# Optimization experiments

Hardware: AMD Instinct MI355X
Metric: run time of the kernel (lower is better)

Reference implementation:

```python
import jax, jax.numpy as jnp
import numpy as np

SLIDING_WINDOW = 512  # matches init kwarg
BLOCK_STRIDE = 32     # tokens per cache page


def setup_inputs() -> dict:
    key = jax.random.key(0)
    k0, k1, k2, k3 = jax.random.split(key, 4)
    B, S, HQ, HKV, D = 2, 2048, 32, 8, 128
    nb = S // BLOCK_STRIDE
    q = jax.random.normal(k0, (B, S, HQ, D), jnp.float32)
    k = jax.random.normal(k1, (B, S, HKV, D), jnp.float32)
    v = jax.random.normal(k2, (B, S, HKV, D), jnp.float32)
    sink = jax.random.normal(k3, (HQ,), jnp.float32)
    cache_state = jnp.zeros((B * nb, 2, HKV, BLOCK_STRIDE, D), jnp.float32)
    seq_block_ids = jnp.arange(B * nb, dtype=jnp.int32).reshape(B, nb)
    return {"q": q, "k": k, "v": v, "cache_state": cache_state,
            "seq_block_ids": seq_block_ids, "sink": sink}


def reference(q, k, v, cache_state, seq_block_ids, sink):
    B, S, HQ, D = q.shape
    HKV = k.shape[2]
    G = HQ // HKV  # GQA group size
    stride = cache_state.shape[3]
    nb = S // stride

    # --- write prefill K/V into the paged cache ---
    # pages laid out [num_pages, k/v, HKV, stride, D]
    k_pg = k.reshape(B, nb, stride, HKV, D).transpose(0, 1, 3, 2, 4).reshape(B * nb, HKV, stride, D)
    v_pg = v.reshape(B, nb, stride, HKV, D).transpose(0, 1, 3, 2, 4).reshape(B * nb, HKV, stride, D)
    ids = seq_block_ids.reshape(-1)
    new_cache = cache_state.at[ids, 0].set(k_pg).at[ids, 1].set(v_pg)

    # --- sliding-window causal attention with sink logits (GQA, no repeat) ---
    scale = 1.0 / np.sqrt(D).astype(np.float32)
    qg = q.reshape(B, S, HKV, G, D)
    # scores: [B, HKV, G, Sq, Sk]
    scores = jnp.einsum('bqhgd,bshd->bhgqs', qg, k) * scale
    i = jnp.arange(S)[:, None]
    j = jnp.arange(S)[None, :]
    allowed = (j <= i) & ((i - j) < SLIDING_WINDOW)  # causal banded mask
    neg = jnp.finfo(scores.dtype).min
    scores = jnp.where(allowed, scores, neg)
    # per-head sink logit appended as extra key column, dropped after softmax
    sink_col = jnp.broadcast_to(sink.reshape(HKV, G)[None, :, :, None, None], (B, HKV, G, S, 1))
    probs = jax.nn.softmax(jnp.concatenate([scores, sink_col], axis=-1), axis=-1)[..., :S]
    out = jnp.einsum('bhgqs,bshd->bqhgd', probs, v).reshape(B, S, HQ, D)
    return out, new_cache
```

## Files before the change

### kernel.cpp

```cpp
#include <hip/hip_runtime.h>
#include <hip/hip_bf16.h>
#include <stdint.h>

#define BB 2
#define SS 2048
#define HQ 32
#define HKV 8
#define DD 128
#define WIN 512

typedef __bf16 bf16x8 __attribute__((ext_vector_type(8)));
typedef __bf16 bf16x4 __attribute__((ext_vector_type(4)));
typedef float f32x4 __attribute__((ext_vector_type(4)));

__device__ __forceinline__ bf16x8 cvt8(float4 a, float4 b, float s) {
  bf16x8 r;
  r[0] = (__bf16)(a.x * s); r[1] = (__bf16)(a.y * s);
  r[2] = (__bf16)(a.z * s); r[3] = (__bf16)(a.w * s);
  r[4] = (__bf16)(b.x * s); r[5] = (__bf16)(b.y * s);
  r[6] = (__bf16)(b.z * s); r[7] = (__bf16)(b.w * s);
  return r;
}

__global__ __launch_bounds__(512, 2) void attn_kernel(
    const float* __restrict__ qg, const float* __restrict__ kg,
    const float* __restrict__ vg, const float* __restrict__ sinkg,
    float* __restrict__ outg)
{
  const int sid = (blockIdx.x & 7) * 64 + (blockIdx.x >> 3);
  const int qtile = sid & 31, hkv = (sid >> 5) & 7, b = sid >> 8;
  const int qb = qtile * 64;
  const int tid = threadIdx.x;
  const int wave = tid >> 6, lane = tid & 63;
  const int wq = wave & 3, wh = wave >> 2;
  const int g = lane >> 4, c = lane & 15;
  const int hq0 = (hkv << 2) + (wh << 1);

  __shared__ __bf16 Kl[2][32 * 128];
  __shared__ __bf16 Vt[2][128 * 40];
  __shared__ __bf16 Pl[16][16 * 40];

  const float LOG2E = 1.4426950408889634f;
  const float scale = 0.08838834764831845f * LOG2E;
  const float THR = 12.0f;
  const int qw = qb + wq * 16;
  const int qrow = qw + c;

  bf16x8 qf[2][4];
  #pragma unroll
  for (int hh = 0; hh < 2; ++hh) {
    const float* qp = qg + (((size_t)b * SS + qrow) * HQ + hq0 + hh) * DD;
    #pragma unroll
    for (int ch = 0; ch < 4; ++ch) {
      float4 a = *(const float4*)(qp + ch * 32 + g * 8);
      float4 b2 = *(const float4*)(qp + ch * 32 + g * 8 + 4);
      qf[hh][ch] = cvt8(a, b2, scale);
    }
  }

  const float sk[2] = {sinkg[hq0] * LOG2E, sinkg[hq0 + 1] * LOG2E};

  float mm[2] = {-1e30f, -1e30f}, ll[2] = {0.f, 0.f};
  f32x4 acc[2][8];
  #pragma unroll
  for (int hh = 0; hh < 2; ++hh)
    #pragma unroll
    for (int i = 0; i < 8; ++i) acc[hh][i] = (f32x4){0.f, 0.f, 0.f, 0.f};

  const int t0 = (qb > (WIN - 1) ? (qb - (WIN - 1)) : 0) >> 5;
  const int t1 = (qb + 63) >> 5;

  const int krow = tid >> 4, kh = tid & 15;
  const int vd = tid & 127, vc4 = tid >> 7;
  const int KSTEP = 32 * HKV * DD;
  const float* kp = kg + (((size_t)b * SS + (t0 << 5) + krow) * HKV + hkv) * DD + kh * 8;
  const float* vp = vg + (((size_t)b * SS + (t0 << 5) + vc4 * 8) * HKV + hkv) * DD + vd;

  float4 ka, ka2; float vr[8];
  auto issue = [&]() {
    ka = *(const float4*)(kp);
    ka2 = *(const float4*)(kp + 4);
    #pragma unroll
    for (int j = 0; j < 8; ++j) vr[j] = vp[(size_t)j * (HKV * DD)];
  };
  auto commit = [&](int buf) {
    *(bf16x8*)((char*)(&Kl[buf][0]) + krow * 256 + ((kh * 16) ^ ((krow & 7) << 4))) =
        cvt8(ka, ka2, 1.f);
    bf16x8 w;
    #pragma unroll
    for (int j = 0; j < 8; ++j) w[j] = (__bf16)vr[j];
    *(bf16x8*)(&Vt[buf][vd * 40 + vc4 * 8]) = w;
  };

  issue();
  commit(0);
  __syncthreads();
  int cur = 0;

  for (int t = t0; t <= t1; ++t) {
    const int kb = t << 5;
    const bool hn = (t < t1);
    if (hn) { kp += KSTEP; vp += KSTEP; issue(); }

    const bool active = !(kb > qw + 15 || kb + 31 < qw - (WIN - 1));
    if (active) {
      const __bf16* Ks = &Kl[cur][0];
      const __bf16* Vs = &Vt[cur][0];

      f32x4 sc0[2] = {{0.f,0.f,0.f,0.f},{0.f,0.f,0.f,0.f}};
      f32x4 sc1[2] = {{0.f,0.f,0.f,0.f},{0.f,0.f,0.f,0.f}};
      #pragma unroll
      for (int ch = 0; ch < 4; ++ch) {
        const int off = (ch * 64 + g * 16) ^ ((c & 7) << 4);
        bf16x8 a0 = *(const bf16x8*)((const char*)Ks + c * 256 + off);
        bf16x8 a1 = *(const bf16x8*)((const char*)Ks + (16 + c) * 256 + off);
        sc0[0] = __builtin_amdgcn_mfma_f32_16x16x32_bf16(a0, qf[0][ch], sc0[0], 0, 0, 0);
        sc1[0] = __builtin_amdgcn_mfma_f32_16x16x32_bf16(a1, qf[0][ch], sc1[0], 0, 0, 0);
        sc0[1] = __builtin_amdgcn_mfma_f32_16x16x32_bf16(a0, qf[1][ch], sc0[1], 0, 0, 0);
        sc1[1] = __builtin_amdgcn_mfma_f32_16x16x32_bf16(a1, qf[1][ch], sc1[1], 0, 0, 0);
      }

      const bool noMask = (kb + 31 <= qw) && (kb >= qw - (WIN - 16));

      #pragma unroll
      for (int hh = 0; hh < 2; ++hh) {
        float p[8];
        #pragma unroll
        for (int r = 0; r < 4; ++r) { p[r] = sc0[hh][r]; p[4 + r] = sc1[hh][r]; }
        if (!noMask) {
          #pragma unroll
          for (int t2 = 0; t2 < 2; ++t2)
            #pragma unroll
            for (int r = 0; r < 4; ++r) {
              const int kk = kb + t2 * 16 + g * 4 + r;
              const bool ok = (kk <= qrow) && (qrow - kk < WIN);
              p[t2 * 4 + r] = ok ? p[t2 * 4 + r] : -1e30f;
            }
        }
        float tmax = p[0];
        #pragma unroll
        for (int j = 1; j < 8; ++j) tmax = fmaxf(tmax, p[j]);
        tmax = fmaxf(tmax, __shfl_xor(tmax, 16));
        tmax = fmaxf(tmax, __shfl_xor(tmax, 32));

        const bool resc = __any(tmax > mm[hh] + THR);
        const float mnew = resc ? fmaxf(mm[hh], tmax) : mm[hh];
        float tsum = 0.f;
        if (noMask) {
          #pragma unroll
          for (int j = 0; j < 8; ++j) { p[j] = exp2f(p[j] - mnew); tsum += p[j]; }
        } else {
          #pragma unroll
          for (int j = 0; j < 8; ++j) {
            const float e = (p[j] > -9e29f) ? exp2f(p[j] - mnew) : 0.f;
            p[j] = e; tsum += e;
          }
        }
        tsum += __shfl_xor(tsum, 16);
        tsum += __shfl_xor(tsum, 32);

        if (resc) {
          const float scl = exp2f(mm[hh] - mnew);
          ll[hh] = ll[hh] * scl + tsum;
          const float f0 = __shfl(scl, g * 4 + 0), f1 = __shfl(scl, g * 4 + 1);
          const float f2 = __shfl(scl, g * 4 + 2), f3 = __shfl(scl, g * 4 + 3);
          #pragma unroll
          for (int dt = 0; dt < 8; ++dt) {
            acc[hh][dt][0] *= f0; acc[hh][dt][1] *= f1;
            acc[hh][dt][2] *= f2; acc[hh][dt][3] *= f3;
          }
          mm[hh] = mnew;
        } else {
          ll[hh] += tsum;
        }

        char* pb = (char*)(&Pl[wave * 2 + hh][0]) + c * 80;
        #pragma unroll
        for (int t2 = 0; t2 < 2; ++t2) {
          bf16x4 w;
          w[0] = (__bf16)p[t2 * 4 + 0]; w[1] = (__bf16)p[t2 * 4 + 1];
          w[2] = (__bf16)p[t2 * 4 + 2]; w[3] = (__bf16)p[t2 * 4 + 3];
          *(bf16x4*)(pb + t2 * 32 + g * 8) = w;
        }
      }

      bf16x8 pa0 = *(bf16x8*)((char*)(&Pl[wave * 2 + 0][0]) + c * 80 + g * 16);
      bf16x8 pa1 = *(bf16x8*)((char*)(&Pl[wave * 2 + 1][0]) + c * 80 + g * 16);
      #pragma unroll
      for (int dt = 0; dt < 8; ++dt) {
        bf16x8 vv = *(const bf16x8*)(Vs + (dt * 16 + c) * 40 + g * 8);
        acc[0][dt] = __builtin_amdgcn_mfma_f32_16x16x32_bf16(pa0, vv, acc[0][dt], 0, 0, 0);
        acc[1][dt] = __builtin_amdgcn_mfma_f32_16x16x32_bf16(pa1, vv, acc[1][dt], 0, 0, 0);
      }
    }

    if (hn) {
      commit(cur ^ 1);
      __syncthreads();
      cur ^= 1;
    }
  }

  #pragma unroll
  for (int hh = 0; hh < 2; ++hh) {
    const float Mf = fmaxf(mm[hh], sk[hh]);
    const float ex = exp2f(mm[hh] - Mf);
    const float denom = ll[hh] * ex + exp2f(sk[hh] - Mf);
    const float fac = ex / denom;
    const float f0 = __shfl(fac, g * 4 + 0), f1 = __shfl(fac, g * 4 + 1);
    const float f2 = __shfl(fac, g * 4 + 2), f3 = __shfl(fac, g * 4 + 3);
    const float fr[4] = {f0, f1, f2, f3};
    #pragma unroll
    for (int dt = 0; dt < 8; ++dt) {
      #pragma unroll
      for (int r = 0; r < 4; ++r) {
        const int row = qw + g * 4 + r;
        outg[(((size_t)b * SS + row) * HQ + hq0 + hh) * DD + dt * 16 + c] = acc[hh][dt][r] * fr[r];
      }
    }
  }
}

__global__ void build_inv(const int* __restrict__ ids, int* __restrict__ inv,
                          int npages, int nslots) {
  const int i = threadIdx.x;
  if (i < npages) inv[i] = -1;
  __syncthreads();
  if (i < nslots) inv[ids[i]] = i;
}

__global__ void page_fill(const float* __restrict__ kg, const float* __restrict__ vg,
                          const float* __restrict__ cache_in, const int* __restrict__ inv,
                          float* __restrict__ cache) {
  const int page = blockIdx.x, half = blockIdx.y;
  const int slot = inv[page];
  float4* d4 = (float4*)cache;
  const size_t dbase = (((size_t)page * 2 + half) * 8) * 1024;
  if (slot >= 0) {
    const int b = slot >> 6, blk = slot & 63;
    const float4* s4 = (const float4*)(half ? vg : kg);
    for (int f = threadIdx.x; f < 8192; f += blockDim.x) {
      const int d = f & 31, s = (f >> 5) & 31, h = f >> 10;
      d4[dbase + (size_t)h * 1024 + s * 32 + d] =
          s4[(((size_t)b * SS + blk * 32 + s) * 8 + h) * 32 + d];
    }
  } else {
    const float4* s4 = (const float4*)cache_in;
    for (int f = threadIdx.x; f < 8192; f += blockDim.x)
      d4[dbase + f] = s4[dbase + f];
  }
}

__global__ void cache_copy(const float* __restrict__ src, float* __restrict__ dst, int n4) {
  const float4* s = (const float4*)src;
  float4* d = (float4*)dst;
  for (int i = blockIdx.x * blockDim.x + threadIdx.x; i < n4; i += gridDim.x * blockDim.x)
    d[i] = s[i];
}
__global__ void cache_scatter(const float* __restrict__ kg, const float* __restrict__ vg,
                              const int* __restrict__ ids, float* __restrict__ cache) {
  const int slot = blockIdx.x;
  const int half = blockIdx.y;
  const int b = slot >> 6, blk = slot & 63;
  const int page = ids[slot];
  const float4* s4 = (const float4*)(half ? vg : kg);
  float4* d4 = (float4*)cache;
  for (int f = threadIdx.x; f < 8192; f += blockDim.x) {
    const int d = f & 31, s = (f >> 5) & 31, h = f >> 10;
    d4[(((size_t)page * 2 + half) * 8 + h) * 1024 + s * 32 + d] =
        s4[(((size_t)b * SS + blk * 32 + s) * 8 + h) * 32 + d];
  }
}

extern "C" void kernel_launch(void* const* d_in, const int* in_sizes, int n_in,
                              void* d_out, int out_size, void* d_ws, size_t ws_size,
                              hipStream_t stream) {
  const float* q = (const float*)d_in[0];
  const float* k = (const float*)d_in[1];
  const float* v = (const float*)d_in[2];
  const float* cache_in = (const float*)d_in[3];
  const int* ids = (const int*)d_in[4];
  const float* sink = (const float*)d_in[5];
  float* out = (float*)d_out;
  float* cache_out = out + (size_t)BB * SS * HQ * DD;

  const int nslots = in_sizes[4];
  const int npages = in_sizes[3] / (2 * HKV * 32 * DD);

  if (ws_size >= (size_t)npages * sizeof(int) && npages <= 1024) {
    int* inv = (int*)d_ws;
    build_inv<<<1, 1024, 0, stream>>>(ids, inv, npages, nslots);
    page_fill<<<dim3(npages, 2), 256, 0, stream>>>(k, v, cache_in, inv, cache_out);
  } else {
    cache_copy<<<4096, 256, 0, stream>>>(cache_in, cache_out, (BB * SS * HKV * DD * 2) / 4);
    cache_scatter<<<dim3(BB * 64, 2), 256, 0, stream>>>(k, v, ids, cache_out);
  }
  attn_kernel<<<512, 512, 0, stream>>>(q, k, v, sink, out);
}
```

Before: 109.9 us.

## Double query tile per block to 128 rows, reuse K/V tiles across two row slabs

```diff
diff --git a/kernel.cpp b/kernel.cpp
--- a/kernel.cpp
+++ b/kernel.cpp
@@ -27,9 +27,9 @@
     const float* __restrict__ vg, const float* __restrict__ sinkg,
     float* __restrict__ outg)
 {
-  const int sid = (blockIdx.x & 7) * 64 + (blockIdx.x >> 3);
-  const int qtile = sid & 31, hkv = (sid >> 5) & 7, b = sid >> 8;
-  const int qb = qtile * 64;
+  const int sid = (blockIdx.x & 7) * 32 + (blockIdx.x >> 3);
+  const int qtile = sid & 15, hkv = (sid >> 4) & 7, b = sid >> 7;
+  const int qb = qtile * 128;
   const int tid = threadIdx.x;
   const int wave = tid >> 6, lane = tid & 63;
   const int wq = wave & 3, wh = wave >> 2;
@@ -38,37 +38,39 @@
 
   __shared__ __bf16 Kl[2][32 * 128];
   __shared__ __bf16 Vt[2][128 * 40];
-  __shared__ __bf16 Pl[16][16 * 40];
+  __shared__ __bf16 Pl[32][16 * 40];
 
   const float LOG2E = 1.4426950408889634f;
   const float scale = 0.08838834764831845f * LOG2E;
   const float THR = 12.0f;
-  const int qw = qb + wq * 16;
-  const int qrow = qw + c;
-
-  bf16x8 qf[2][4];
+  const int qw_lo = qb + wq * 32;
+
+  bf16x8 qf[4][4];
   #pragma unroll
-  for (int hh = 0; hh < 2; ++hh) {
-    const float* qp = qg + (((size_t)b * SS + qrow) * HQ + hq0 + hh) * DD;
-    #pragma unroll
-    for (int ch = 0; ch < 4; ++ch) {
-      float4 a = *(const float4*)(qp + ch * 32 + g * 8);
-      float4 b2 = *(const float4*)(qp + ch * 32 + g * 8 + 4);
-      qf[hh][ch] = cvt8(a, b2, scale);
-    }
-  }
+  for (int rs = 0; rs < 2; ++rs)
+    #pragma unroll
+    for (int hh = 0; hh < 2; ++hh) {
+      const float* qp = qg + (((size_t)b * SS + qw_lo + rs * 16 + c) * HQ + hq0 + hh) * DD;
+      #pragma unroll
+      for (int ch = 0; ch < 4; ++ch) {
+        float4 a = *(const float4*)(qp + ch * 32 + g * 8);
+        float4 b2 = *(const float4*)(qp + ch * 32 + g * 8 + 4);
+        qf[rs * 2 + hh][ch] = cvt8(a, b2, scale);
+      }
+    }
 
   const float sk[2] = {sinkg[hq0] * LOG2E, sinkg[hq0 + 1] * LOG2E};
 
-  float mm[2] = {-1e30f, -1e30f}, ll[2] = {0.f, 0.f};
-  f32x4 acc[2][8];
+  float mm[4] = {-1e30f, -1e30f, -1e30f, -1e30f};
+  float ll[4] = {0.f, 0.f, 0.f, 0.f};
+  f32x4 acc[4][8];
   #pragma unroll
-  for (int hh = 0; hh < 2; ++hh)
-    #pragma unroll
-    for (int i = 0; i < 8; ++i) acc[hh][i] = (f32x4){0.f, 0.f, 0.f, 0.f};
+  for (int mi = 0; mi < 4; ++mi)
+    #pragma unroll
+    for (int i = 0; i < 8; ++i) acc[mi][i] = (f32x4){0.f, 0.f, 0.f, 0.f};
 
   const int t0 = (qb > (WIN - 1) ? (qb - (WIN - 1)) : 0) >> 5;
-  const int t1 = (qb + 63) >> 5;
+  const int t1 = (qb + 127) >> 5;
 
   const int krow = tid >> 4, kh = tid & 15;
   const int vd = tid & 127, vc4 = tid >> 7;
@@ -102,96 +104,111 @@
     const bool hn = (t < t1);
     if (hn) { kp += KSTEP; vp += KSTEP; issue(); }
 
-    const bool active = !(kb > qw + 15 || kb + 31 < qw - (WIN - 1));
-    if (active) {
+    const bool activeW = !(kb > qw_lo + 31 || kb + 31 < qw_lo - (WIN - 1));
+    if (activeW) {
       const __bf16* Ks = &Kl[cur][0];
       const __bf16* Vs = &Vt[cur][0];
 
-      f32x4 sc0[2] = {{0.f,0.f,0.f,0.f},{0.f,0.f,0.f,0.f}};
-      f32x4 sc1[2] = {{0.f,0.f,0.f,0.f},{0.f,0.f,0.f,0.f}};
-      #pragma unroll
-      for (int ch = 0; ch < 4; ++ch) {
-        const int off = (ch * 64 + g * 16) ^ ((c & 7) << 4);
-        bf16x8 a0 = *(const bf16x8*)((const char*)Ks + c * 256 + off);
-        bf16x8 a1 = *(const bf16x8*)((const char*)Ks + (16 + c) * 256 + off);
-        sc0[0] = __builtin_amdgcn_mfma_f32_16x16x32_bf16(a0, qf[0][ch], sc0[0], 0, 0, 0);
-        sc1[0] = __builtin_amdgcn_mfma_f32_16x16x32_bf16(a1, qf[0][ch], sc1[0], 0, 0, 0);
-        sc0[1] = __builtin_amdgcn_mfma_f32_16x16x32_bf16(a0, qf[1][ch], sc0[1], 0, 0, 0);
-        sc1[1] = __builtin_amdgcn_mfma_f32_16x16x32_bf16(a1, qf[1][ch], sc1[1], 0, 0, 0);
-      }
-
-      const bool noMask = (kb + 31 <= qw) && (kb >= qw - (WIN - 16));
-
-      #pragma unroll
-      for (int hh = 0; hh < 2; ++hh) {
-        float p[8];
+      #pragma unroll
+      for (int rs = 0; rs < 2; ++rs) {
+        const int qw = qw_lo + rs * 16;
+        const int qrow = qw + c;
+
+        f32x4 s0[2] = {{0.f,0.f,0.f,0.f},{0.f,0.f,0.f,0.f}};
+        f32x4 s1[2] = {{0.f,0.f,0.f,0.f},{0.f,0.f,0.f,0.f}};
+        __builtin_amdgcn_s_setprio(1);
         #pragma unroll
-        for (int r = 0; r < 4; ++r) { p[r] = sc0[hh][r]; p[4 + r] = sc1[hh][r]; }
-        if (!noMask) {
+        for (int ch = 0; ch < 4; ++ch) {
+          const int off = (ch * 64 + g * 16) ^ ((c & 7) << 4);
+          bf16x8 a0 = *(const bf16x8*)((const char*)Ks + c * 256 + off);
+          bf16x8 a1 = *(const bf16x8*)((const char*)Ks + (16 + c) * 256 + off);
+          s0[0] = __builtin_amdgcn_mfma_f32_16x16x32_bf16(a0, qf[rs * 2 + 0][ch], s0[0], 0, 0, 0);
+          s1[0] = __builtin_amdgcn_mfma_f32_16x16x32_bf16(a1, qf[rs * 2 + 0][ch], s1[0], 0, 0, 0);
+          s0[1] = __builtin_amdgcn_mfma_f32_16x16x32_bf16(a0, qf[rs * 2 + 1][ch], s0[1], 0, 0, 0);
+          s1[1] = __builtin_amdgcn_mfma_f32_16x16x32_bf16(a1, qf[rs * 2 + 1][ch], s1[1], 0, 0, 0);
+        }
+        __builtin_amdgcn_s_setprio(0);
+
+        const bool noMask = (kb + 31 <= qw) && (kb >= qw - (WIN - 16));
+
+        #pragma unroll
+        for (int hh = 0; hh < 2; ++hh) {
+          const int mi = rs * 2 + hh;
+          float p[8];
           #pragma unroll
-          for (int t2 = 0; t2 < 2; ++t2)
+          for (int r = 0; r < 4; ++r) { p[r] = s0[hh][r]; p[4 + r] = s1[hh][r]; }
+          if (!noMask) {
             #pragma unroll
-            for (int r = 0; r < 4; ++r) {
-              const int kk = kb + t2 * 16 + g * 4 + r;
-              const bool ok = (kk <= qrow) && (qrow - kk < WIN);
-              p[t2 * 4 + r] = ok ? p[t2 * 4 + r] : -1e30f;
+            for (int t2 = 0; t2 < 2; ++t2)
+              #pragma unroll
+              for (int r = 0; r < 4; ++r) {
+                const int kk = kb + t2 * 16 + g * 4 + r;
+                const bool ok = (kk <= qrow) && (qrow - kk < WIN);
+                p[t2 * 4 + r] = ok ? p[t2 * 4 + r] : -1e30f;
+              }
+          }
+          float tmax = p[0];
+          #pragma unroll
+          for (int j = 1; j < 8; ++j) tmax = fmaxf(tmax, p[j]);
+          tmax = fmaxf(tmax, __shfl_xor(tmax, 16));
+          tmax = fmaxf(tmax, __shfl_xor(tmax, 32));
+
+          const bool resc = __any(tmax > mm[mi] + THR);
+          const float mnew = resc ? fmaxf(mm[mi], tmax) : mm[mi];
+          float tsum = 0.f;
+          if (noMask) {
+            #pragma unroll
+            for (int j = 0; j < 8; ++j) { p[j] = exp2f(p[j] - mnew); tsum += p[j]; }
+          } else {
+            #pragma unroll
+            for (int j = 0; j < 8; ++j) {
+              const float e = (p[j] > -9e29f) ? exp2f(p[j] - mnew) : 0.f;
+              p[j] = e; tsum += e;
             }
-        }
-        float tmax = p[0];
-        #pragma unroll
-        for (int j = 1; j < 8; ++j) tmax = fmaxf(tmax, p[j]);
-        tmax = fmaxf(tmax, __shfl_xor(tmax, 16));
-        tmax = fmaxf(tmax, __shfl_xor(tmax, 32));
-
-        const bool resc = __any(tmax > mm[hh] + THR);
-        const float mnew = resc ? fmaxf(mm[hh], tmax) : mm[hh];
-        float tsum = 0.f;
-        if (noMask) {
+          }
+          tsum += __shfl_xor(tsum, 16);
+          tsum += __shfl_xor(tsum, 32);
+
+          if (resc) {
+            const float scl = exp2f(mm[mi] - mnew);
+            ll[mi] = ll[mi] * scl + tsum;
+            const float f0 = __shfl(scl, g * 4 + 0), f1 = __shfl(scl, g * 4 + 1);
+            const float f2 = __shfl(scl, g * 4 + 2), f3 = __shfl(scl, g * 4 + 3);
+            #pragma unroll
+            for (int dt = 0; dt < 8; ++dt) {
+              acc[mi][dt][0] *= f0; acc[mi][dt][1] *= f1;
+              acc[mi][dt][2] *= f2; acc[mi][dt][3] *= f3;
+            }
+            mm[mi] = mnew;
+          } else {
+            ll[mi] += tsum;
+          }
+
+          char* pb = (char*)(&Pl[wave * 4 + mi][0]) + c * 80;
           #pragma unroll
-          for (int j = 0; j < 8; ++j) { p[j] = exp2f(p[j] - mnew); tsum += p[j]; }
-        } else {
-          #pragma unroll
-          for (int j = 0; j < 8; ++j) {
-            const float e = (p[j] > -9e29f) ? exp2f(p[j] - mnew) : 0.f;
-            p[j] = e; tsum += e;
+          for (int t2 = 0; t2 < 2; ++t2) {
+            bf16x4 w;
+            w[0] = (__bf16)p[t2 * 4 + 0]; w[1] = (__bf16)p[t2 * 4 + 1];
+            w[2] = (__bf16)p[t2 * 4 + 2]; w[3] = (__bf16)p[t2 * 4 + 3];
+            *(bf16x4*)(pb + t2 * 32 + g * 8) = w;
           }
         }
-        tsum += __shfl_xor(tsum, 16);
-        tsum += __shfl_xor(tsum, 32);
-
-        if (resc) {
-          const float scl = exp2f(mm[hh] - mnew);
-          ll[hh] = ll[hh] * scl + tsum;
-          const float f0 = __shfl(scl, g * 4 + 0), f1 = __shfl(scl, g * 4 + 1);
-          const float f2 = __shfl(scl, g * 4 + 2), f3 = __shfl(scl, g * 4 + 3);
-          #pragma unroll
-          for (int dt = 0; dt < 8; ++dt) {
-            acc[hh][dt][0] *= f0; acc[hh][dt][1] *= f1;
-            acc[hh][dt][2] *= f2; acc[hh][dt][3] *= f3;
-          }
-          mm[hh] = mnew;
-        } else {
-          ll[hh] += tsum;
-        }
-
-        char* pb = (char*)(&Pl[wave * 2 + hh][0]) + c * 80;
-        #pragma unroll
-        for (int t2 = 0; t2 < 2; ++t2) {
-          bf16x4 w;
-          w[0] = (__bf16)p[t2 * 4 + 0]; w[1] = (__bf16)p[t2 * 4 + 1];
-          w[2] = (__bf16)p[t2 * 4 + 2]; w[3] = (__bf16)p[t2 * 4 + 3];
-          *(bf16x4*)(pb + t2 * 32 + g * 8) = w;
-        }
       }
 
-      bf16x8 pa0 = *(bf16x8*)((char*)(&Pl[wave * 2 + 0][0]) + c * 80 + g * 16);
-      bf16x8 pa1 = *(bf16x8*)((char*)(&Pl[wave * 2 + 1][0]) + c * 80 + g * 16);
+      bf16x8 pa[4];
+      #pragma unroll
+      for (int mi = 0; mi < 4; ++mi)
+        pa[mi] = *(bf16x8*)((char*)(&Pl[wave * 4 + mi][0]) + c * 80 + g * 16);
+      __builtin_amdgcn_s_setprio(1);
       #pragma unroll
       for (int dt = 0; dt < 8; ++dt) {
         bf16x8 vv = *(const bf16x8*)(Vs + (dt * 16 + c) * 40 + g * 8);
-        acc[0][dt] = __builtin_amdgcn_mfma_f32_16x16x32_bf16(pa0, vv, acc[0][dt], 0, 0, 0);
-        acc[1][dt] = __builtin_amdgcn_mfma_f32_16x16x32_bf16(pa1, vv, acc[1][dt], 0, 0, 0);
+        acc[0][dt] = __builtin_amdgcn_mfma_f32_16x16x32_bf16(pa[0], vv, acc[0][dt], 0, 0, 0);
+        acc[1][dt] = __builtin_amdgcn_mfma_f32_16x16x32_bf16(pa[1], vv, acc[1][dt], 0, 0, 0);
+        acc[2][dt] = __builtin_amdgcn_mfma_f32_16x16x32_bf16(pa[2], vv, acc[2][dt], 0, 0, 0);
+        acc[3][dt] = __builtin_amdgcn_mfma_f32_16x16x32_bf16(pa[3], vv, acc[3][dt], 0, 0, 0);
       }
+      __builtin_amdgcn_s_setprio(0);
     }
 
     if (hn) {
@@ -202,10 +219,11 @@
   }
 
   #pragma unroll
-  for (int hh = 0; hh < 2; ++hh) {
-    const float Mf = fmaxf(mm[hh], sk[hh]);
-    const float ex = exp2f(mm[hh] - Mf);
-    const float denom = ll[hh] * ex + exp2f(sk[hh] - Mf);
+  for (int mi = 0; mi < 4; ++mi) {
+    const int rs = mi >> 1, hh = mi & 1;
+    const float Mf = fmaxf(mm[mi], sk[hh]);
+    const float ex = exp2f(mm[mi] - Mf);
+    const float denom = ll[mi] * ex + exp2f(sk[hh] - Mf);
     const float fac = ex / denom;
     const float f0 = __shfl(fac, g * 4 + 0), f1 = __shfl(fac, g * 4 + 1);
     const float f2 = __shfl(fac, g * 4 + 2), f3 = __shfl(fac, g * 4 + 3);
@@ -214,8 +232,8 @@
     for (int dt = 0; dt < 8; ++dt) {
       #pragma unroll
       for (int r = 0; r < 4; ++r) {
-        const int row = qw + g * 4 + r;
-        outg[(((size_t)b * SS + row) * HQ + hq0 + hh) * DD + dt * 16 + c] = acc[hh][dt][r] * fr[r];
+        const int row = qw_lo + rs * 16 + g * 4 + r;
+        outg[(((size_t)b * SS + row) * HQ + hq0 + hh) * DD + dt * 16 + c] = acc[mi][dt][r] * fr[r];
       }
     }
   }
@@ -295,5 +313,5 @@
     cache_copy<<<4096, 256, 0, stream>>>(cache_in, cache_out, (BB * SS * HKV * DD * 2) / 4);
     cache_scatter<<<dim3(BB * 64, 2), 256, 0, stream>>>(k, v, ids, cache_out);
   }
-  attn_kernel<<<512, 512, 0, stream>>>(q, k, v, sink, out);
-}
+  attn_kernel<<<256, 512, 0, stream>>>(q, k, v, sink, out);
+}
```

New measurement: 169.3 us. 1.54x slower.

## Transpose PV MFMA operands, vectorize output stores, reorder block schedule, add setprio

Applied to the files above, without the earlier changes.

```diff
diff --git a/kernel.cpp b/kernel.cpp
--- a/kernel.cpp
+++ b/kernel.cpp
@@ -27,8 +27,10 @@
     const float* __restrict__ vg, const float* __restrict__ sinkg,
     float* __restrict__ outg)
 {
-  const int sid = (blockIdx.x & 7) * 64 + (blockIdx.x >> 3);
-  const int qtile = sid & 31, hkv = (sid >> 5) & 7, b = sid >> 8;
+  const int col = (blockIdx.x & 7) + 8 * ((blockIdx.x >> 3) & 1);
+  const int rank = blockIdx.x >> 4;
+  const int qtile = rank < 24 ? rank + 8 : 31 - rank;
+  const int hkv = col & 7, b = col >> 3;
   const int qb = qtile * 64;
   const int tid = threadIdx.x;
   const int wave = tid >> 6, lane = tid & 63;
@@ -107,18 +109,20 @@
       const __bf16* Ks = &Kl[cur][0];
       const __bf16* Vs = &Vt[cur][0];
 
-      f32x4 sc0[2] = {{0.f,0.f,0.f,0.f},{0.f,0.f,0.f,0.f}};
-      f32x4 sc1[2] = {{0.f,0.f,0.f,0.f},{0.f,0.f,0.f,0.f}};
+      f32x4 s0[2] = {{0.f,0.f,0.f,0.f},{0.f,0.f,0.f,0.f}};
+      f32x4 s1[2] = {{0.f,0.f,0.f,0.f},{0.f,0.f,0.f,0.f}};
+      __builtin_amdgcn_s_setprio(1);
       #pragma unroll
       for (int ch = 0; ch < 4; ++ch) {
         const int off = (ch * 64 + g * 16) ^ ((c & 7) << 4);
         bf16x8 a0 = *(const bf16x8*)((const char*)Ks + c * 256 + off);
         bf16x8 a1 = *(const bf16x8*)((const char*)Ks + (16 + c) * 256 + off);
-        sc0[0] = __builtin_amdgcn_mfma_f32_16x16x32_bf16(a0, qf[0][ch], sc0[0], 0, 0, 0);
-        sc1[0] = __builtin_amdgcn_mfma_f32_16x16x32_bf16(a1, qf[0][ch], sc1[0], 0, 0, 0);
-        sc0[1] = __builtin_amdgcn_mfma_f32_16x16x32_bf16(a0, qf[1][ch], sc0[1], 0, 0, 0);
-        sc1[1] = __builtin_amdgcn_mfma_f32_16x16x32_bf16(a1, qf[1][ch], sc1[1], 0, 0, 0);
+        s0[0] = __builtin_amdgcn_mfma_f32_16x16x32_bf16(a0, qf[0][ch], s0[0], 0, 0, 0);
+        s1[0] = __builtin_amdgcn_mfma_f32_16x16x32_bf16(a1, qf[0][ch], s1[0], 0, 0, 0);
+        s0[1] = __builtin_amdgcn_mfma_f32_16x16x32_bf16(a0, qf[1][ch], s0[1], 0, 0, 0);
+        s1[1] = __builtin_amdgcn_mfma_f32_16x16x32_bf16(a1, qf[1][ch], s1[1], 0, 0, 0);
       }
+      __builtin_amdgcn_s_setprio(0);
 
       const bool noMask = (kb + 31 <= qw) && (kb >= qw - (WIN - 16));
 
@@ -126,7 +130,7 @@
       for (int hh = 0; hh < 2; ++hh) {
         float p[8];
         #pragma unroll
-        for (int r = 0; r < 4; ++r) { p[r] = sc0[hh][r]; p[4 + r] = sc1[hh][r]; }
+        for (int r = 0; r < 4; ++r) { p[r] = s0[hh][r]; p[4 + r] = s1[hh][r]; }
         if (!noMask) {
           #pragma unroll
           for (int t2 = 0; t2 < 2; ++t2)
@@ -162,12 +166,10 @@
         if (resc) {
           const float scl = exp2f(mm[hh] - mnew);
           ll[hh] = ll[hh] * scl + tsum;
-          const float f0 = __shfl(scl, g * 4 + 0), f1 = __shfl(scl, g * 4 + 1);
-          const float f2 = __shfl(scl, g * 4 + 2), f3 = __shfl(scl, g * 4 + 3);
           #pragma unroll
           for (int dt = 0; dt < 8; ++dt) {
-            acc[hh][dt][0] *= f0; acc[hh][dt][1] *= f1;
-            acc[hh][dt][2] *= f2; acc[hh][dt][3] *= f3;
+            acc[hh][dt][0] *= scl; acc[hh][dt][1] *= scl;
+            acc[hh][dt][2] *= scl; acc[hh][dt][3] *= scl;
           }
           mm[hh] = mnew;
         } else {
@@ -186,12 +188,14 @@
 
       bf16x8 pa0 = *(bf16x8*)((char*)(&Pl[wave * 2 + 0][0]) + c * 80 + g * 16);
       bf16x8 pa1 = *(bf16x8*)((char*)(&Pl[wave * 2 + 1][0]) + c * 80 + g * 16);
+      __builtin_amdgcn_s_setprio(1);
       #pragma unroll
       for (int dt = 0; dt < 8; ++dt) {
         bf16x8 vv = *(const bf16x8*)(Vs + (dt * 16 + c) * 40 + g * 8);
-        acc[0][dt] = __builtin_amdgcn_mfma_f32_16x16x32_bf16(pa0, vv, acc[0][dt], 0, 0, 0);
-        acc[1][dt] = __builtin_amdgcn_mfma_f32_16x16x32_bf16(pa1, vv, acc[1][dt], 0, 0, 0);
+        acc[0][dt] = __builtin_amdgcn_mfma_f32_16x16x32_bf16(vv, pa0, acc[0][dt], 0, 0, 0);
+        acc[1][dt] = __builtin_amdgcn_mfma_f32_16x16x32_bf16(vv, pa1, acc[1][dt], 0, 0, 0);
       }
+      __builtin_amdgcn_s_setprio(0);
     }
 
     if (hn) {
@@ -207,16 +211,13 @@
     const float ex = exp2f(mm[hh] - Mf);
     const float denom = ll[hh] * ex + exp2f(sk[hh] - Mf);
     const float fac = ex / denom;
-    const float f0 = __shfl(fac, g * 4 + 0), f1 = __shfl(fac, g * 4 + 1);
-    const float f2 = __shfl(fac, g * 4 + 2), f3 = __shfl(fac, g * 4 + 3);
-    const float fr[4] = {f0, f1, f2, f3};
+    float* orow = outg + (((size_t)b * SS + qw + c) * HQ + hq0 + hh) * DD;
     #pragma unroll
     for (int dt = 0; dt < 8; ++dt) {
-      #pragma unroll
-      for (int r = 0; r < 4; ++r) {
-        const int row = qw + g * 4 + r;
-        outg[(((size_t)b * SS + row) * HQ + hq0 + hh) * DD + dt * 16 + c] = acc[hh][dt][r] * fr[r];
-      }
+      float4 o;
+      o.x = acc[hh][dt][0] * fac; o.y = acc[hh][dt][1] * fac;
+      o.z = acc[hh][dt][2] * fac; o.w = acc[hh][dt][3] * fac;
+      *(float4*)(orow + dt * 16 + 4 * g) = o;
     }
   }
 }
```

New measurement: 112.8 us. +2.6%, slower.
